# Kernel tuning notes

Hardware: AMD Instinct MI355X
Metric: run time of the kernel (lower is better)

## Reference

```python
import jax, jax.numpy as jnp
import numpy as np

NB, D, H, DH, DHID = 12, 512, 8, 64, 1024  # n_blocks, d_model, n_heads, d_head, d_hidden
B, S = 2, 2048
EPS = 1e-5


def _ln(x, g, b):
    m = jnp.mean(x, axis=-1, keepdims=True)
    v = jnp.mean(jnp.square(x - m), axis=-1, keepdims=True)
    return (x - m) / jnp.sqrt(v + EPS) * g + b


def setup_inputs() -> dict:
    key = jax.random.key(0)
    ks = jax.random.split(key, 8)
    s = 0.02
    f32 = jnp.float32
    return {
        "X": jax.random.normal(ks[0], (B, S, D), f32),
        "qkv_w": jax.random.normal(ks[1], (NB, D, 3 * D), f32) * s,
        "qkv_b": jnp.zeros((NB, 3 * D), f32),
        "fc_w": jax.random.normal(ks[2], (NB, D, D), f32) * s,
        "fc_b": jnp.zeros((NB, D), f32),
        "ln1_g": jnp.ones((NB, D), f32),
        "ln1_b": jnp.zeros((NB, D), f32),
        "w1": jax.random.normal(ks[3], (NB, D, DHID), f32) * s,
        "b1": jnp.zeros((NB, DHID), f32),
        "w2": jax.random.normal(ks[4], (NB, DHID, D), f32) * s,
        "b2": jnp.zeros((NB, D), f32),
        "ln2_g": jnp.ones((NB, D), f32),
        "ln2_b": jnp.zeros((NB, D), f32),
    }


def reference(X, qkv_w, qkv_b, fc_w, fc_b, ln1_g, ln1_b, w1, b1, w2, b2, ln2_g, ln2_b):
    scale = 1.0 / np.sqrt(D)  # NOTE: original scales by 1/sqrt(d_model), not 1/sqrt(d_head)

    def body(x, p):
        qw, qb, fw, fb, g1, be1, w1_, bb1, w2_, bb2, g2, be2 = p
        b, s, _ = x.shape
        # qkv -> [b, h, s, 3*dh]; split per-head AFTER head reshape (as in chunk(dim=-1))
        ctx = (x @ qw + qb).reshape(b, s, H, 3 * DH).transpose(0, 2, 1, 3)
        q, k, v = jnp.split(ctx, 3, axis=-1)  # each [b, h, s, dh]
        attn = jax.nn.softmax(jnp.einsum('bhqd,bhkd->bhqk', q, k) * scale, axis=-1)
        o = jnp.einsum('bhqk,bhkd->bhqd', attn, v).transpose(0, 2, 1, 3).reshape(b, s, D)
        x = x + (o @ fw + fb)                      # residual + attn out proj (dropout=0)
        h = jax.nn.relu(_ln(x, g1, be1) @ w1_ + bb1)
        x = x + (h @ w2_ + bb2)                    # residual + MLP
        return _ln(x, g2, be2), None

    out, _ = jax.lax.scan(
        body, X,
        (qkv_w, qkv_b, fc_w, fc_b, ln1_g, ln1_b, w1, b1, w2, b2, ln2_g, ln2_b))
    return out
```

## Files before the change

kernel.cpp:

```cpp
#include <hip/hip_runtime.h>

typedef unsigned short ushort_t;
typedef __attribute__((ext_vector_type(8))) short bf16x8;
typedef __attribute__((ext_vector_type(4))) float f32x4;
typedef __attribute__((ext_vector_type(4))) unsigned short us4;

#define DEV __device__ __forceinline__

DEV ushort_t f2b(float f) {
    union { float f; unsigned u; } x; x.f = f;
    unsigned r = (x.u + 0x7fffu + ((x.u >> 16) & 1u)) >> 16;
    return (ushort_t)r;
}

DEV unsigned cvt_pk_bf16(float lo, float hi) {
    unsigned r;
    asm("v_cvt_pk_bf16_f32 %0, %1, %2" : "=v"(r) : "v"(lo), "v"(hi));
    return r;
}

typedef void __attribute__((address_space(1)))* gp1;
typedef void __attribute__((address_space(3)))* sp3;
DEV void gload_lds16(const void* g, void* l) {
    __builtin_amdgcn_global_load_lds((gp1)g, (sp3)l, 16, 0, 0);
}

__global__ __launch_bounds__(256) void transpose_cvt(
    const float* __restrict__ in, ushort_t* __restrict__ out, int K, int N)
{
    __shared__ float tile[32][33];
    const int nb = blockIdx.z;
    const float* src = in + (size_t)nb * K * N;
    ushort_t* dst = out + (size_t)nb * K * N;
    const int n0 = blockIdx.x * 32, k0 = blockIdx.y * 32;
    const int tx = threadIdx.x & 31, ty = threadIdx.x >> 5;
#pragma unroll
    for (int i = 0; i < 32; i += 8)
        tile[ty + i][tx] = src[(size_t)(k0 + ty + i) * N + n0 + tx];
    __syncthreads();
#pragma unroll
    for (int i = 0; i < 32; i += 8)
        dst[(size_t)(n0 + ty + i) * K + k0 + tx] = f2b(tile[tx][ty + i]);
}

__global__ __launch_bounds__(256) void init_x(
    const float* __restrict__ X, float* __restrict__ xf, ushort_t* __restrict__ xb)
{
    const int i = blockIdx.x * 256 + threadIdx.x;
    const float4 v = ((const float4*)X)[i];
    ((float4*)xf)[i] = v;
    us4 o = { f2b(v.x), f2b(v.y), f2b(v.z), f2b(v.w) };
    ((us4*)xb)[i] = o;
}

enum { EPI_QKV = 0, EPI_RESF32 = 1, EPI_RELUB = 2 };

template<int EPI>
__global__ __launch_bounds__(256, 2) void gemm64(
    const ushort_t* __restrict__ A, const ushort_t* __restrict__ Wt,
    const float* __restrict__ bias, const float* __restrict__ resid,
    float* __restrict__ Cf, ushort_t* __restrict__ Cb,
    ushort_t* __restrict__ Oq, ushort_t* __restrict__ Ok, ushort_t* __restrict__ Ov,
    int M, int N, int K)
{
    __shared__ __align__(16) ushort_t lA[2][64 * 64];
    __shared__ __align__(16) ushort_t lB[2][128 * 64];
    const int nbm = M >> 6;
    const int bm = blockIdx.x % nbm;
    const int bn = blockIdx.x / nbm;
    const int tid = threadIdx.x, lane = tid & 63, w = tid >> 6;
    const int l15 = lane & 15, l4 = lane >> 4;

    f32x4 acc[4][2];
#pragma unroll
    for (int i = 0; i < 4; i++)
#pragma unroll
        for (int j = 0; j < 2; j++) { f32x4 z = {0.f, 0.f, 0.f, 0.f}; acc[i][j] = z; }

    const int srow = tid >> 3;
    const int sch = tid & 7;
    const int swch = sch ^ (srow & 7);
    const ushort_t* Asrc0 = A  + (size_t)(bm * 64 + srow) * K + swch * 8;
    const ushort_t* Asrc1 = A  + (size_t)(bm * 64 + srow + 32) * K + swch * 8;
    const ushort_t* Bsrc0 = Wt + (size_t)(bn * 128 + srow) * K + swch * 8;
    const ushort_t* Bsrc1 = Wt + (size_t)(bn * 128 + srow + 32) * K + swch * 8;
    const ushort_t* Bsrc2 = Wt + (size_t)(bn * 128 + srow + 64) * K + swch * 8;
    const ushort_t* Bsrc3 = Wt + (size_t)(bn * 128 + srow + 96) * K + swch * 8;
    char* lAc = (char*)lA;
    char* lBc = (char*)lB;

#define GE_STAGE(buf, k0) do {                                            \
        gload_lds16(Asrc0 + (k0), lAc + (buf) * 8192  + w * 1024);        \
        gload_lds16(Asrc1 + (k0), lAc + (buf) * 8192  + 4096 + w * 1024); \
        gload_lds16(Bsrc0 + (k0), lBc + (buf) * 16384 + w * 1024);        \
        gload_lds16(Bsrc1 + (k0), lBc + (buf) * 16384 + 4096 + w * 1024); \
        gload_lds16(Bsrc2 + (k0), lBc + (buf) * 16384 + 8192 + w * 1024); \
        gload_lds16(Bsrc3 + (k0), lBc + (buf) * 16384 + 12288 + w * 1024);\
    } while (0)

    GE_STAGE(0, 0);
    __syncthreads();

    const int nIt = K >> 6;
    int cur = 0;
    for (int it = 0; it < nIt; ++it) {
        if (it + 1 < nIt) GE_STAGE(cur ^ 1, (it + 1) * 64);
#pragma unroll
        for (int ks = 0; ks < 2; ks++) {
            bf16x8 af[4], bfr[2];
#pragma unroll
            for (int i = 0; i < 4; i++) {
                const int row = i * 16 + l15;
                af[i] = *(const bf16x8*)(lAc + cur * 8192 + row * 128 +
                                         (((ks * 4 + l4) ^ (row & 7)) << 4));
            }
#pragma unroll
            for (int j = 0; j < 2; j++) {
                const int row = w * 32 + j * 16 + l15;
                bfr[j] = *(const bf16x8*)(lBc + cur * 16384 + row * 128 +
                                          (((ks * 4 + l4) ^ (row & 7)) << 4));
            }
#pragma unroll
            for (int i = 0; i < 4; i++)
#pragma unroll
                for (int j = 0; j < 2; j++)
                    acc[i][j] = __builtin_amdgcn_mfma_f32_16x16x32_bf16(af[i], bfr[j], acc[i][j], 0, 0, 0);
        }
        __syncthreads();
        cur ^= 1;
    }
#undef GE_STAGE

    const int mbase = bm * 64;
    const int nbase = bn * 128 + w * 32;
#pragma unroll
    for (int j = 0; j < 2; j++) {
        const int nf16 = nbase + j * 16;
        const float bv = bias[nf16 + l15];
        if constexpr (EPI == EPI_QKV) {
            const int head = nf16 / 192;
            const int rem = nf16 - head * 192;
            const int part = rem >> 6;
            const int dh = (rem & 63) + l15;
#pragma unroll
            for (int i = 0; i < 4; i++) {
                const int m0 = mbase + i * 16 + l4 * 4;
#pragma unroll
                for (int r = 0; r < 4; r++) {
                    const int m = m0 + r;
                    const int b = m >> 11, s = m & 2047;
                    const float v = acc[i][j][r] + bv;
                    if (part == 0)
                        Oq[((size_t)(b * 8 + head) * 2048 + s) * 64 + dh] = f2b(v);
                    else if (part == 1)
                        Ok[((size_t)(b * 8 + head) * 2048 + s) * 64 + dh] = f2b(v);
                    else
                        Ov[((size_t)(b * 8 + head) * 64 + dh) * 2048 + s] = f2b(v);
                }
            }
        } else if constexpr (EPI == EPI_RESF32) {
#pragma unroll
            for (int i = 0; i < 4; i++) {
                const int m0 = mbase + i * 16 + l4 * 4;
#pragma unroll
                for (int r = 0; r < 4; r++) {
                    const size_t idx = (size_t)(m0 + r) * N + nf16 + l15;
                    Cf[idx] = acc[i][j][r] + bv + resid[idx];
                }
            }
        } else {
#pragma unroll
            for (int i = 0; i < 4; i++) {
                const int m0 = mbase + i * 16 + l4 * 4;
#pragma unroll
                for (int r = 0; r < 4; r++) {
                    const size_t idx = (size_t)(m0 + r) * N + nf16 + l15;
                    const float v = acc[i][j][r] + bv;
                    Cb[idx] = f2b(v > 0.f ? v : 0.f);
                }
            }
        }
    }
}

__global__ __launch_bounds__(256, 2) void flash_attn3(
    const ushort_t* __restrict__ Q, const ushort_t* __restrict__ Kg,
    const ushort_t* __restrict__ Vg, ushort_t* __restrict__ O, float sl2)
{
    __shared__ __align__(16) ushort_t lK[2][64 * 64];
    __shared__ __align__(16) ushort_t lV[2][64 * 64];
    __shared__ __align__(16) ushort_t lP[4][16 * 64];

    const int id = blockIdx.x;
    const int xcd = id & 7, rest = id >> 3;
    const int qt = rest & 31;
    const int bh = xcd + ((rest >> 5) << 3);
    const int tid = threadIdx.x, lane = tid & 63, w = tid >> 6;
    const int l15 = lane & 15, l4 = lane >> 4;
    const int qrow0 = qt * 64 + w * 16;

    const ushort_t* Qb = Q + ((size_t)bh * 2048 + qrow0) * 64;
    bf16x8 qf[2];
#pragma unroll
    for (int ks = 0; ks < 2; ks++)
        qf[ks] = *(const bf16x8*)(Qb + l15 * 64 + ks * 32 + l4 * 8);

    const ushort_t* Kbase = Kg + (size_t)bh * 2048 * 64;
    const ushort_t* Vbase = Vg + (size_t)bh * 64 * 2048;

    float m_run = -100000.f;
    float l_run = 0.f;
    f32x4 oacc[4];
#pragma unroll
    for (int nd = 0; nd < 4; nd++) { f32x4 z = {0.f, 0.f, 0.f, 0.f}; oacc[nd] = z; }

    char* lKc = (char*)lK;
    char* lVc = (char*)lV;
    char* myP = (char*)(lP[w]);

    const int srow8 = lane >> 3;
    const int sch = lane & 7;

#define FA_STAGE(buf, kt) do {                                              \
        const int row0_ = w * 16 + srow8;                                   \
        const int sc0_ = sch ^ (row0_ & 7);                                 \
        gload_lds16(Kbase + (size_t)((kt) * 64 + row0_) * 64 + sc0_ * 8,    \
                    lKc + (buf) * 8192 + w * 2048);                         \
        gload_lds16(Vbase + (size_t)row0_ * 2048 + (kt) * 64 + sc0_ * 8,    \
                    lVc + (buf) * 8192 + w * 2048);                         \
        gload_lds16(Kbase + (size_t)((kt) * 64 + row0_ + 8) * 64 + sc0_ * 8,\
                    lKc + (buf) * 8192 + w * 2048 + 1024);                  \
        gload_lds16(Vbase + (size_t)(row0_ + 8) * 2048 + (kt) * 64 + sc0_ * 8,\
                    lVc + (buf) * 8192 + w * 2048 + 1024);                  \
    } while (0)

    FA_STAGE(0, 0);
    __syncthreads();

    int cur = 0;
    for (int kt = 0; kt < 32; kt++) {
        if (kt < 31) FA_STAGE(cur ^ 1, kt + 1);

        f32x4 sc4[4];
#pragma unroll
        for (int nf = 0; nf < 4; nf++) { f32x4 z = {0.f, 0.f, 0.f, 0.f}; sc4[nf] = z; }
#pragma unroll
        for (int nf = 0; nf < 4; nf++) {
            const int krow = nf * 16 + l15;
#pragma unroll
            for (int ks = 0; ks < 2; ks++) {
                const bf16x8 kf = *(const bf16x8*)(lKc + cur * 8192 + krow * 128 +
                                                   (((ks * 4 + l4) ^ (krow & 7)) << 4));
                sc4[nf] = __builtin_amdgcn_mfma_f32_16x16x32_bf16(kf, qf[ks], sc4[nf], 0, 0, 0);
            }
        }

        float mx = fmaxf(fmaxf(sc4[0][0], sc4[0][1]), fmaxf(sc4[0][2], sc4[0][3]));
#pragma unroll
        for (int nf = 1; nf < 4; nf++)
            mx = fmaxf(mx, fmaxf(fmaxf(sc4[nf][0], sc4[nf][1]),
                                 fmaxf(sc4[nf][2], sc4[nf][3])));
        mx = fmaxf(mx, __shfl_xor(mx, 16));
        mx = fmaxf(mx, __shfl_xor(mx, 32));

        const int need = (mx > m_run + 125.f) ? 1 : 0;
        if (__any(need)) {
            const float mn = fmaxf(m_run, mx);
            const float corr = exp2f((m_run - mn) * sl2);
            m_run = mn;
            l_run *= corr;
            float cr[4];
#pragma unroll
            for (int r = 0; r < 4; r++) cr[r] = __shfl(corr, l4 * 4 + r);
#pragma unroll
            for (int nd = 0; nd < 4; nd++)
#pragma unroll
                for (int r = 0; r < 4; r++) oacc[nd][r] *= cr[r];
        }

        const float msl = m_run * sl2;
        float ps = 0.f;
#pragma unroll
        for (int nf = 0; nf < 4; nf++)
#pragma unroll
            for (int r = 0; r < 4; r++) {
                const float p = exp2f(sc4[nf][r] * sl2 - msl);
                sc4[nf][r] = p;
                ps += p;
            }
        l_run += ps;

#pragma unroll
        for (int nf = 0; nf < 4; nf++)
#pragma unroll
            for (int h = 0; h < 2; h++) {
                const unsigned pw = cvt_pk_bf16(sc4[nf][2 * h], sc4[nf][2 * h + 1]);
                const int colb = nf * 32 + l4 * 8 + h * 4;
                *(unsigned*)(myP + l15 * 128 + (colb ^ ((l15 & 7) << 4))) = pw;
            }
        __asm__ volatile("" ::: "memory");

        bf16x8 pa[2];
#pragma unroll
        for (int ks = 0; ks < 2; ks++)
            pa[ks] = *(const bf16x8*)(myP + l15 * 128 +
                                      ((ks * 64 + l4 * 16) ^ ((l15 & 7) << 4)));
#pragma unroll
        for (int ks = 0; ks < 2; ks++)
#pragma unroll
            for (int nd = 0; nd < 4; nd++) {
                const int vrow = nd * 16 + l15;
                const bf16x8 vf = *(const bf16x8*)(lVc + cur * 8192 + vrow * 128 +
                                                   (((ks * 4 + l4) ^ (vrow & 7)) << 4));
                oacc[nd] = __builtin_amdgcn_mfma_f32_16x16x32_bf16(pa[ks], vf, oacc[nd], 0, 0, 0);
            }
        __syncthreads();
        cur ^= 1;
    }
#undef FA_STAGE

    l_run += __shfl_xor(l_run, 16);
    l_run += __shfl_xor(l_run, 32);
    const int bq = bh >> 3, hh = bh & 7;
#pragma unroll
    for (int r = 0; r < 4; r++) {
        const float lr = __shfl(l_run, l4 * 4 + r);
        const float inv = 1.f / lr;
        const int s = qrow0 + l4 * 4 + r;
#pragma unroll
        for (int nd = 0; nd < 4; nd++)
            O[((size_t)(bq * 2048 + s)) * 512 + hh * 64 + nd * 16 + l15] = f2b(oacc[nd][r] * inv);
    }
}

__global__ __launch_bounds__(256) void layernorm512(
    const float* X, const float* __restrict__ g, const float* __restrict__ bta,
    ushort_t* __restrict__ Yb, float* Yf)
{
    const int row = blockIdx.x * 4 + (threadIdx.x >> 6);
    const int lane = threadIdx.x & 63;
    const float4* xp = (const float4*)(X + (size_t)row * 512);
    const float4 v0 = xp[lane];
    const float4 v1 = xp[lane + 64];
    float s = v0.x + v0.y + v0.z + v0.w + v1.x + v1.y + v1.z + v1.w;
    float s2 = v0.x * v0.x + v0.y * v0.y + v0.z * v0.z + v0.w * v0.w
             + v1.x * v1.x + v1.y * v1.y + v1.z * v1.z + v1.w * v1.w;
#pragma unroll
    for (int m = 1; m < 64; m <<= 1) { s += __shfl_xor(s, m); s2 += __shfl_xor(s2, m); }
    const float mean = s * (1.f / 512.f);
    const float inv = rsqrtf(s2 * (1.f / 512.f) - mean * mean + 1e-5f);
    const float4 g0 = ((const float4*)g)[lane], g1 = ((const float4*)g)[lane + 64];
    const float4 b0 = ((const float4*)bta)[lane], b1 = ((const float4*)bta)[lane + 64];
    float4 y0, y1;
    y0.x = (v0.x - mean) * inv * g0.x + b0.x;
    y0.y = (v0.y - mean) * inv * g0.y + b0.y;
    y0.z = (v0.z - mean) * inv * g0.z + b0.z;
    y0.w = (v0.w - mean) * inv * g0.w + b0.w;
    y1.x = (v1.x - mean) * inv * g1.x + b1.x;
    y1.y = (v1.y - mean) * inv * g1.y + b1.y;
    y1.z = (v1.z - mean) * inv * g1.z + b1.z;
    y1.w = (v1.w - mean) * inv * g1.w + b1.w;
    if (Yf) {
        ((float4*)(Yf + (size_t)row * 512))[lane] = y0;
        ((float4*)(Yf + (size_t)row * 512))[lane + 64] = y1;
    }
    us4 o0 = { f2b(y0.x), f2b(y0.y), f2b(y0.z), f2b(y0.w) };
    us4 o1 = { f2b(y1.x), f2b(y1.y), f2b(y1.z), f2b(y1.w) };
    ((us4*)(Yb + (size_t)row * 512))[lane] = o0;
    ((us4*)(Yb + (size_t)row * 512))[lane + 64] = o1;
}

extern "C" void kernel_launch(void* const* d_in, const int* in_sizes, int n_in,
                              void* d_out, int out_size, void* d_ws, size_t ws_size,
                              hipStream_t stream)
{
    (void)in_sizes; (void)n_in; (void)out_size; (void)ws_size;
    const float* X     = (const float*)d_in[0];
    const float* qkv_w = (const float*)d_in[1];
    const float* qkv_b = (const float*)d_in[2];
    const float* fc_w  = (const float*)d_in[3];
    const float* fc_b  = (const float*)d_in[4];
    const float* ln1_g = (const float*)d_in[5];
    const float* ln1_b = (const float*)d_in[6];
    const float* w1    = (const float*)d_in[7];
    const float* b1    = (const float*)d_in[8];
    const float* w2    = (const float*)d_in[9];
    const float* b2    = (const float*)d_in[10];
    const float* ln2_g = (const float*)d_in[11];
    const float* ln2_b = (const float*)d_in[12];

    char* ws = (char*)d_ws;
    size_t off = 0;
    auto alloc = [&](size_t bytes) -> char* {
        char* p = ws + off;
        off += (bytes + 255) & ~(size_t)255;
        return p;
    };
    ushort_t* qkvw_t = (ushort_t*)alloc(12ull * 1536 * 512 * 2);
    ushort_t* fcw_t  = (ushort_t*)alloc(12ull * 512 * 512 * 2);
    ushort_t* w1_t   = (ushort_t*)alloc(12ull * 512 * 1024 * 2);
    ushort_t* w2_t   = (ushort_t*)alloc(12ull * 1024 * 512 * 2);
    float*    xf     = (float*)   alloc(4096ull * 512 * 4);
    ushort_t* xb     = (ushort_t*)alloc(4096ull * 512 * 2);
    ushort_t* qb     = (ushort_t*)alloc(16ull * 2048 * 64 * 2);
    ushort_t* kb     = (ushort_t*)alloc(16ull * 2048 * 64 * 2);
    ushort_t* vt     = (ushort_t*)alloc(16ull * 64 * 2048 * 2);
    ushort_t* ob     = (ushort_t*)alloc(4096ull * 512 * 2);
    ushort_t* y1     = (ushort_t*)alloc(4096ull * 512 * 2);
    ushort_t* hbuf   = (ushort_t*)alloc(4096ull * 1024 * 2);

    transpose_cvt<<<dim3(48, 16, 12), 256, 0, stream>>>(qkv_w, qkvw_t, 512, 1536);
    transpose_cvt<<<dim3(16, 16, 12), 256, 0, stream>>>(fc_w, fcw_t, 512, 512);
    transpose_cvt<<<dim3(32, 16, 12), 256, 0, stream>>>(w1, w1_t, 512, 1024);
    transpose_cvt<<<dim3(16, 32, 12), 256, 0, stream>>>(w2, w2_t, 1024, 512);
    init_x<<<2048, 256, 0, stream>>>(X, xf, xb);

    const float sl2 = (float)(0.044194173824159216 * 1.4426950408889634);
    for (int nb = 0; nb < 12; nb++) {
        gemm64<EPI_QKV><<<64 * 12, 256, 0, stream>>>(
            xb, qkvw_t + (size_t)nb * 1536 * 512, qkv_b + nb * 1536,
            nullptr, nullptr, nullptr, qb, kb, vt, 4096, 1536, 512);
        flash_attn3<<<512, 256, 0, stream>>>(qb, kb, vt, ob, sl2);
        gemm64<EPI_RESF32><<<64 * 4, 256, 0, stream>>>(
            ob, fcw_t + (size_t)nb * 512 * 512, fc_b + nb * 512,
            xf, xf, nullptr, nullptr, nullptr, nullptr, 4096, 512, 512);
        layernorm512<<<1024, 256, 0, stream>>>(xf, ln1_g + nb * 512, ln1_b + nb * 512, y1, nullptr);
        gemm64<EPI_RELUB><<<64 * 8, 256, 0, stream>>>(
            y1, w1_t + (size_t)nb * 1024 * 512, b1 + nb * 1024,
            nullptr, nullptr, hbuf, nullptr, nullptr, nullptr, 4096, 1024, 512);
        gemm64<EPI_RESF32><<<64 * 4, 256, 0, stream>>>(
            hbuf, w2_t + (size_t)nb * 1024 * 512, b2 + nb * 512,
            xf, xf, nullptr, nullptr, nullptr, nullptr, 4096, 512, 1024);
        layernorm512<<<1024, 256, 0, stream>>>(xf, ln2_g + nb * 512, ln2_b + nb * 512, xb,
                                               nb == 11 ? (float*)d_out : xf);
    }
}
```

Before: 1.337 ms.

## Split-K residual GEMMs with atomics and double query tiles per wave in attention

The out-projection and MLP-down GEMMs now split K in two across blocks and accumulate into the residual buffer with atomicAdd, with the bias added only by the first split. This doubles the number of blocks for the narrow N=512 GEMMs. Flash attention is restructured so each of 2 waves processes 32 query rows, reusing each K/V LDS fragment for two MFMAs, and gains setprio hints around the matmul sections. The V-transpose store in the QKV epilogue is vectorized. The trade-offs are atomic traffic and nondeterministic summation order, plus fewer waves per attention block.

```diff
diff --git a/kernel.cpp b/kernel.cpp
--- a/kernel.cpp
+++ b/kernel.cpp
@@ -53,12 +53,12 @@
     ((us4*)xb)[i] = o;
 }
 
-enum { EPI_QKV = 0, EPI_RESF32 = 1, EPI_RELUB = 2 };
-
-template<int EPI>
+enum { EPI_QKV = 0, EPI_RESADD = 1, EPI_RELUB = 2 };
+
+template<int EPI, int KSPL>
 __global__ __launch_bounds__(256, 2) void gemm64(
     const ushort_t* __restrict__ A, const ushort_t* __restrict__ Wt,
-    const float* __restrict__ bias, const float* __restrict__ resid,
+    const float* __restrict__ bias,
     float* __restrict__ Cf, ushort_t* __restrict__ Cb,
     ushort_t* __restrict__ Oq, ushort_t* __restrict__ Ok, ushort_t* __restrict__ Ov,
     int M, int N, int K)
@@ -66,8 +66,13 @@
     __shared__ __align__(16) ushort_t lA[2][64 * 64];
     __shared__ __align__(16) ushort_t lB[2][128 * 64];
     const int nbm = M >> 6;
-    const int bm = blockIdx.x % nbm;
-    const int bn = blockIdx.x / nbm;
+    const int nbn = N >> 7;
+    int bid = blockIdx.x;
+    const int bm = bid % nbm; bid /= nbm;
+    const int bn = bid % nbn;
+    const int kh = bid / nbn;
+    const int Keff = K / KSPL;
+    const int kbase = kh * Keff;
     const int tid = threadIdx.x, lane = tid & 63, w = tid >> 6;
     const int l15 = lane & 15, l4 = lane >> 4;
 
@@ -80,12 +85,12 @@
     const int srow = tid >> 3;
     const int sch = tid & 7;
     const int swch = sch ^ (srow & 7);
-    const ushort_t* Asrc0 = A  + (size_t)(bm * 64 + srow) * K + swch * 8;
-    const ushort_t* Asrc1 = A  + (size_t)(bm * 64 + srow + 32) * K + swch * 8;
-    const ushort_t* Bsrc0 = Wt + (size_t)(bn * 128 + srow) * K + swch * 8;
-    const ushort_t* Bsrc1 = Wt + (size_t)(bn * 128 + srow + 32) * K + swch * 8;
-    const ushort_t* Bsrc2 = Wt + (size_t)(bn * 128 + srow + 64) * K + swch * 8;
-    const ushort_t* Bsrc3 = Wt + (size_t)(bn * 128 + srow + 96) * K + swch * 8;
+    const ushort_t* Asrc0 = A  + (size_t)(bm * 64 + srow) * K + kbase + swch * 8;
+    const ushort_t* Asrc1 = A  + (size_t)(bm * 64 + srow + 32) * K + kbase + swch * 8;
+    const ushort_t* Bsrc0 = Wt + (size_t)(bn * 128 + srow) * K + kbase + swch * 8;
+    const ushort_t* Bsrc1 = Wt + (size_t)(bn * 128 + srow + 32) * K + kbase + swch * 8;
+    const ushort_t* Bsrc2 = Wt + (size_t)(bn * 128 + srow + 64) * K + kbase + swch * 8;
+    const ushort_t* Bsrc3 = Wt + (size_t)(bn * 128 + srow + 96) * K + kbase + swch * 8;
     char* lAc = (char*)lA;
     char* lBc = (char*)lB;
 
@@ -101,7 +106,7 @@
     GE_STAGE(0, 0);
     __syncthreads();
 
-    const int nIt = K >> 6;
+    const int nIt = Keff >> 6;
     int cur = 0;
     for (int it = 0; it < nIt; ++it) {
         if (it + 1 < nIt) GE_STAGE(cur ^ 1, (it + 1) * 64);
@@ -145,27 +150,30 @@
 #pragma unroll
             for (int i = 0; i < 4; i++) {
                 const int m0 = mbase + i * 16 + l4 * 4;
-#pragma unroll
-                for (int r = 0; r < 4; r++) {
-                    const int m = m0 + r;
-                    const int b = m >> 11, s = m & 2047;
-                    const float v = acc[i][j][r] + bv;
-                    if (part == 0)
-                        Oq[((size_t)(b * 8 + head) * 2048 + s) * 64 + dh] = f2b(v);
-                    else if (part == 1)
-                        Ok[((size_t)(b * 8 + head) * 2048 + s) * 64 + dh] = f2b(v);
-                    else
-                        Ov[((size_t)(b * 8 + head) * 64 + dh) * 2048 + s] = f2b(v);
+                const int b = m0 >> 11, s0 = m0 & 2047;
+                if (part == 2) {
+                    us4 pv;
+#pragma unroll
+                    for (int r = 0; r < 4; r++) pv[r] = f2b(acc[i][j][r] + bv);
+                    *(us4*)(&Ov[((size_t)(b * 8 + head) * 64 + dh) * 2048 + s0]) = pv;
+                } else {
+                    ushort_t* dst = (part == 0) ? Oq : Ok;
+#pragma unroll
+                    for (int r = 0; r < 4; r++)
+                        dst[((size_t)(b * 8 + head) * 2048 + s0 + r) * 64 + dh] =
+                            f2b(acc[i][j][r] + bv);
                 }
             }
-        } else if constexpr (EPI == EPI_RESF32) {
+        } else if constexpr (EPI == EPI_RESADD) {
+            const float badd = (kh == 0) ? bv : 0.f;
 #pragma unroll
             for (int i = 0; i < 4; i++) {
                 const int m0 = mbase + i * 16 + l4 * 4;
 #pragma unroll
                 for (int r = 0; r < 4; r++) {
                     const size_t idx = (size_t)(m0 + r) * N + nf16 + l15;
-                    Cf[idx] = acc[i][j][r] + bv + resid[idx];
+                    if constexpr (KSPL == 1) Cf[idx] += acc[i][j][r] + badd;
+                    else atomicAdd(&Cf[idx], acc[i][j][r] + badd);
                 }
             }
         } else {
@@ -183,13 +191,13 @@
     }
 }
 
-__global__ __launch_bounds__(256, 2) void flash_attn3(
+__global__ __launch_bounds__(128, 2) void flash_attn4(
     const ushort_t* __restrict__ Q, const ushort_t* __restrict__ Kg,
     const ushort_t* __restrict__ Vg, ushort_t* __restrict__ O, float sl2)
 {
     __shared__ __align__(16) ushort_t lK[2][64 * 64];
     __shared__ __align__(16) ushort_t lV[2][64 * 64];
-    __shared__ __align__(16) ushort_t lP[4][16 * 64];
+    __shared__ __align__(16) ushort_t lP[2][32 * 64];
 
     const int id = blockIdx.x;
     const int xcd = id & 7, rest = id >> 3;
@@ -197,42 +205,42 @@
     const int bh = xcd + ((rest >> 5) << 3);
     const int tid = threadIdx.x, lane = tid & 63, w = tid >> 6;
     const int l15 = lane & 15, l4 = lane >> 4;
-    const int qrow0 = qt * 64 + w * 16;
+    const int qrow0 = qt * 64 + w * 32;
 
     const ushort_t* Qb = Q + ((size_t)bh * 2048 + qrow0) * 64;
-    bf16x8 qf[2];
-#pragma unroll
-    for (int ks = 0; ks < 2; ks++)
-        qf[ks] = *(const bf16x8*)(Qb + l15 * 64 + ks * 32 + l4 * 8);
+    bf16x8 qf[2][2];
+#pragma unroll
+    for (int qi = 0; qi < 2; qi++)
+#pragma unroll
+        for (int ks = 0; ks < 2; ks++)
+            qf[qi][ks] = *(const bf16x8*)(Qb + (qi * 16 + l15) * 64 + ks * 32 + l4 * 8);
 
     const ushort_t* Kbase = Kg + (size_t)bh * 2048 * 64;
     const ushort_t* Vbase = Vg + (size_t)bh * 64 * 2048;
 
-    float m_run = -100000.f;
-    float l_run = 0.f;
-    f32x4 oacc[4];
-#pragma unroll
-    for (int nd = 0; nd < 4; nd++) { f32x4 z = {0.f, 0.f, 0.f, 0.f}; oacc[nd] = z; }
+    float m_run[2] = { -100000.f, -100000.f };
+    float l_run[2] = { 0.f, 0.f };
+    f32x4 oacc[2][4];
+#pragma unroll
+    for (int qi = 0; qi < 2; qi++)
+#pragma unroll
+        for (int nd = 0; nd < 4; nd++) { f32x4 z = {0.f, 0.f, 0.f, 0.f}; oacc[qi][nd] = z; }
 
     char* lKc = (char*)lK;
     char* lVc = (char*)lV;
     char* myP = (char*)(lP[w]);
 
-    const int srow8 = lane >> 3;
-    const int sch = lane & 7;
-
-#define FA_STAGE(buf, kt) do {                                              \
-        const int row0_ = w * 16 + srow8;                                   \
-        const int sc0_ = sch ^ (row0_ & 7);                                 \
-        gload_lds16(Kbase + (size_t)((kt) * 64 + row0_) * 64 + sc0_ * 8,    \
-                    lKc + (buf) * 8192 + w * 2048);                         \
-        gload_lds16(Vbase + (size_t)row0_ * 2048 + (kt) * 64 + sc0_ * 8,    \
-                    lVc + (buf) * 8192 + w * 2048);                         \
-        gload_lds16(Kbase + (size_t)((kt) * 64 + row0_ + 8) * 64 + sc0_ * 8,\
-                    lKc + (buf) * 8192 + w * 2048 + 1024);                  \
-        gload_lds16(Vbase + (size_t)(row0_ + 8) * 2048 + (kt) * 64 + sc0_ * 8,\
-                    lVc + (buf) * 8192 + w * 2048 + 1024);                  \
-    } while (0)
+    const int srow0 = w * 32 + (lane >> 3);
+    const int swch = (lane & 7) ^ (srow0 & 7);
+
+#define FA_STAGE(buf, kt) do {                                                   \
+        _Pragma("unroll")                                                        \
+        for (int i_ = 0; i_ < 4; i_++) {                                         \
+            gload_lds16(Kbase + (size_t)((kt) * 64 + srow0 + i_ * 8) * 64 + swch * 8, \
+                        lKc + (buf) * 8192 + w * 4096 + i_ * 1024);              \
+            gload_lds16(Vbase + (size_t)(srow0 + i_ * 8) * 2048 + (kt) * 64 + swch * 8, \
+                        lVc + (buf) * 8192 + w * 4096 + i_ * 1024);              \
+        } } while (0)
 
     FA_STAGE(0, 0);
     __syncthreads();
@@ -241,9 +249,12 @@
     for (int kt = 0; kt < 32; kt++) {
         if (kt < 31) FA_STAGE(cur ^ 1, kt + 1);
 
-        f32x4 sc4[4];
-#pragma unroll
-        for (int nf = 0; nf < 4; nf++) { f32x4 z = {0.f, 0.f, 0.f, 0.f}; sc4[nf] = z; }
+        f32x4 sc[2][4];
+#pragma unroll
+        for (int qi = 0; qi < 2; qi++)
+#pragma unroll
+            for (int nf = 0; nf < 4; nf++) { f32x4 z = {0.f, 0.f, 0.f, 0.f}; sc[qi][nf] = z; }
+        __builtin_amdgcn_s_setprio(1);
 #pragma unroll
         for (int nf = 0; nf < 4; nf++) {
             const int krow = nf * 16 + l15;
@@ -251,60 +262,84 @@
             for (int ks = 0; ks < 2; ks++) {
                 const bf16x8 kf = *(const bf16x8*)(lKc + cur * 8192 + krow * 128 +
                                                    (((ks * 4 + l4) ^ (krow & 7)) << 4));
-                sc4[nf] = __builtin_amdgcn_mfma_f32_16x16x32_bf16(kf, qf[ks], sc4[nf], 0, 0, 0);
-            }
-        }
-
-        float mx = fmaxf(fmaxf(sc4[0][0], sc4[0][1]), fmaxf(sc4[0][2], sc4[0][3]));
-#pragma unroll
-        for (int nf = 1; nf < 4; nf++)
-            mx = fmaxf(mx, fmaxf(fmaxf(sc4[nf][0], sc4[nf][1]),
-                                 fmaxf(sc4[nf][2], sc4[nf][3])));
-        mx = fmaxf(mx, __shfl_xor(mx, 16));
-        mx = fmaxf(mx, __shfl_xor(mx, 32));
-
-        const int need = (mx > m_run + 125.f) ? 1 : 0;
+                sc[0][nf] = __builtin_amdgcn_mfma_f32_16x16x32_bf16(kf, qf[0][ks], sc[0][nf], 0, 0, 0);
+                sc[1][nf] = __builtin_amdgcn_mfma_f32_16x16x32_bf16(kf, qf[1][ks], sc[1][nf], 0, 0, 0);
+            }
+        }
+        __builtin_amdgcn_s_setprio(0);
+
+        float mx[2];
+#pragma unroll
+        for (int qi = 0; qi < 2; qi++) {
+            float m0 = fmaxf(fmaxf(sc[qi][0][0], sc[qi][0][1]),
+                             fmaxf(sc[qi][0][2], sc[qi][0][3]));
+#pragma unroll
+            for (int nf = 1; nf < 4; nf++)
+                m0 = fmaxf(m0, fmaxf(fmaxf(sc[qi][nf][0], sc[qi][nf][1]),
+                                     fmaxf(sc[qi][nf][2], sc[qi][nf][3])));
+            m0 = fmaxf(m0, __shfl_xor(m0, 16));
+            m0 = fmaxf(m0, __shfl_xor(m0, 32));
+            mx[qi] = m0;
+        }
+        const int need = (mx[0] > m_run[0] + 125.f) | (mx[1] > m_run[1] + 125.f);
         if (__any(need)) {
-            const float mn = fmaxf(m_run, mx);
-            const float corr = exp2f((m_run - mn) * sl2);
-            m_run = mn;
-            l_run *= corr;
-            float cr[4];
-#pragma unroll
-            for (int r = 0; r < 4; r++) cr[r] = __shfl(corr, l4 * 4 + r);
-#pragma unroll
-            for (int nd = 0; nd < 4; nd++)
-#pragma unroll
-                for (int r = 0; r < 4; r++) oacc[nd][r] *= cr[r];
-        }
-
-        const float msl = m_run * sl2;
-        float ps = 0.f;
-#pragma unroll
-        for (int nf = 0; nf < 4; nf++)
-#pragma unroll
-            for (int r = 0; r < 4; r++) {
-                const float p = exp2f(sc4[nf][r] * sl2 - msl);
-                sc4[nf][r] = p;
-                ps += p;
-            }
-        l_run += ps;
-
-#pragma unroll
-        for (int nf = 0; nf < 4; nf++)
-#pragma unroll
-            for (int h = 0; h < 2; h++) {
-                const unsigned pw = cvt_pk_bf16(sc4[nf][2 * h], sc4[nf][2 * h + 1]);
-                const int colb = nf * 32 + l4 * 8 + h * 4;
-                *(unsigned*)(myP + l15 * 128 + (colb ^ ((l15 & 7) << 4))) = pw;
-            }
+#pragma unroll
+            for (int qi = 0; qi < 2; qi++) {
+                const float mn = fmaxf(m_run[qi], mx[qi]);
+                const float corr = exp2f((m_run[qi] - mn) * sl2);
+                m_run[qi] = mn;
+                l_run[qi] *= corr;
+                float cr[4];
+#pragma unroll
+                for (int r = 0; r < 4; r++) cr[r] = __shfl(corr, l4 * 4 + r);
+#pragma unroll
+                for (int nd = 0; nd < 4; nd++)
+#pragma unroll
+                    for (int r = 0; r < 4; r++) oacc[qi][nd][r] *= cr[r];
+            }
+        }
+#pragma unroll
+        for (int qi = 0; qi < 2; qi++) {
+            const float msl = m_run[qi] * sl2;
+            float ps = 0.f;
+#pragma unroll
+            for (int nf = 0; nf < 4; nf++)
+#pragma unroll
+                for (int r = 0; r < 4; r++) {
+                    const float p = exp2f(sc[qi][nf][r] * sl2 - msl);
+                    sc[qi][nf][r] = p;
+                    ps += p;
+                }
+            l_run[qi] += ps;
+        }
+
+        const int hh0 = (l15 >> 3) & 1;
+#pragma unroll
+        for (int qi = 0; qi < 2; qi++) {
+            const int rowP = qi * 16 + l15;
+            char* rp = myP + rowP * 128;
+            const int swz = (l15 & 7) << 4;
+#pragma unroll
+            for (int nf = 0; nf < 4; nf++) {
+                const unsigned pw0 = cvt_pk_bf16(sc[qi][nf][0], sc[qi][nf][1]);
+                const unsigned pw1 = cvt_pk_bf16(sc[qi][nf][2], sc[qi][nf][3]);
+                const unsigned wA = hh0 ? pw1 : pw0;
+                const unsigned wB = hh0 ? pw0 : pw1;
+                const int cbase = nf * 32 + l4 * 8;
+                *(unsigned*)(rp + ((cbase + hh0 * 4) ^ swz)) = wA;
+                *(unsigned*)(rp + ((cbase + (1 - hh0) * 4) ^ swz)) = wB;
+            }
+        }
         __asm__ volatile("" ::: "memory");
 
-        bf16x8 pa[2];
-#pragma unroll
-        for (int ks = 0; ks < 2; ks++)
-            pa[ks] = *(const bf16x8*)(myP + l15 * 128 +
-                                      ((ks * 64 + l4 * 16) ^ ((l15 & 7) << 4)));
+        bf16x8 pa[2][2];
+#pragma unroll
+        for (int qi = 0; qi < 2; qi++)
+#pragma unroll
+            for (int ks = 0; ks < 2; ks++)
+                pa[qi][ks] = *(const bf16x8*)(myP + (qi * 16 + l15) * 128 +
+                                              ((ks * 64 + l4 * 16) ^ ((l15 & 7) << 4)));
+        __builtin_amdgcn_s_setprio(1);
 #pragma unroll
         for (int ks = 0; ks < 2; ks++)
 #pragma unroll
@@ -312,24 +347,31 @@
                 const int vrow = nd * 16 + l15;
                 const bf16x8 vf = *(const bf16x8*)(lVc + cur * 8192 + vrow * 128 +
                                                    (((ks * 4 + l4) ^ (vrow & 7)) << 4));
-                oacc[nd] = __builtin_amdgcn_mfma_f32_16x16x32_bf16(pa[ks], vf, oacc[nd], 0, 0, 0);
-            }
+                oacc[0][nd] = __builtin_amdgcn_mfma_f32_16x16x32_bf16(pa[0][ks], vf, oacc[0][nd], 0, 0, 0);
+                oacc[1][nd] = __builtin_amdgcn_mfma_f32_16x16x32_bf16(pa[1][ks], vf, oacc[1][nd], 0, 0, 0);
+            }
+        __builtin_amdgcn_s_setprio(0);
         __syncthreads();
         cur ^= 1;
     }
 #undef FA_STAGE
 
-    l_run += __shfl_xor(l_run, 16);
-    l_run += __shfl_xor(l_run, 32);
     const int bq = bh >> 3, hh = bh & 7;
 #pragma unroll
-    for (int r = 0; r < 4; r++) {
-        const float lr = __shfl(l_run, l4 * 4 + r);
-        const float inv = 1.f / lr;
-        const int s = qrow0 + l4 * 4 + r;
-#pragma unroll
-        for (int nd = 0; nd < 4; nd++)
-            O[((size_t)(bq * 2048 + s)) * 512 + hh * 64 + nd * 16 + l15] = f2b(oacc[nd][r] * inv);
+    for (int qi = 0; qi < 2; qi++) {
+        float lr = l_run[qi];
+        lr += __shfl_xor(lr, 16);
+        lr += __shfl_xor(lr, 32);
+#pragma unroll
+        for (int r = 0; r < 4; r++) {
+            const float lv = __shfl(lr, l4 * 4 + r);
+            const float inv = 1.f / lv;
+            const int s = qrow0 + qi * 16 + l4 * 4 + r;
+#pragma unroll
+            for (int nd = 0; nd < 4; nd++)
+                O[((size_t)(bq * 2048 + s)) * 512 + hh * 64 + nd * 16 + l15] =
+                    f2b(oacc[qi][nd][r] * inv);
+        }
     }
 }
 
@@ -417,20 +459,20 @@
 
     const float sl2 = (float)(0.044194173824159216 * 1.4426950408889634);
     for (int nb = 0; nb < 12; nb++) {
-        gemm64<EPI_QKV><<<64 * 12, 256, 0, stream>>>(
+        gemm64<EPI_QKV, 1><<<64 * 12, 256, 0, stream>>>(
             xb, qkvw_t + (size_t)nb * 1536 * 512, qkv_b + nb * 1536,
-            nullptr, nullptr, nullptr, qb, kb, vt, 4096, 1536, 512);
-        flash_attn3<<<512, 256, 0, stream>>>(qb, kb, vt, ob, sl2);
-        gemm64<EPI_RESF32><<<64 * 4, 256, 0, stream>>>(
+            nullptr, nullptr, qb, kb, vt, 4096, 1536, 512);
+        flash_attn4<<<512, 128, 0, stream>>>(qb, kb, vt, ob, sl2);
+        gemm64<EPI_RESADD, 2><<<64 * 4 * 2, 256, 0, stream>>>(
             ob, fcw_t + (size_t)nb * 512 * 512, fc_b + nb * 512,
-            xf, xf, nullptr, nullptr, nullptr, nullptr, 4096, 512, 512);
+            xf, nullptr, nullptr, nullptr, nullptr, 4096, 512, 512);
         layernorm512<<<1024, 256, 0, stream>>>(xf, ln1_g + nb * 512, ln1_b + nb * 512, y1, nullptr);
-        gemm64<EPI_RELUB><<<64 * 8, 256, 0, stream>>>(
+        gemm64<EPI_RELUB, 1><<<64 * 8, 256, 0, stream>>>(
             y1, w1_t + (size_t)nb * 1024 * 512, b1 + nb * 1024,
-            nullptr, nullptr, hbuf, nullptr, nullptr, nullptr, 4096, 1024, 512);
-        gemm64<EPI_RESF32><<<64 * 4, 256, 0, stream>>>(
+            nullptr, hbuf, nullptr, nullptr, nullptr, 4096, 1024, 512);
+        gemm64<EPI_RESADD, 2><<<64 * 4 * 2, 256, 0, stream>>>(
             hbuf, w2_t + (size_t)nb * 1024 * 512, b2 + nb * 512,
-            xf, xf, nullptr, nullptr, nullptr, nullptr, 4096, 512, 1024);
+            xf, nullptr, nullptr, nullptr, nullptr, 4096, 512, 1024);
         layernorm512<<<1024, 256, 0, stream>>>(xf, ln2_g + nb * 512, ln2_b + nb * 512, xb,
                                                nb == 11 ? (float*)d_out : xf);
     }
```

Result: slower. 1.747 ms (+30.6%).

## Split attention KV range with combine pass, use 128x128 GEMM tiles for QKV/FC1

Applied to the files above, without the earlier changes.

Attention now splits the KV sequence in two halves across twice as many blocks, writes fp32 partial outputs plus running max and sum, and merges them in a new combine kernel. The QKV and first MLP GEMMs move to a 128x128 tile kernel with 4x4 MFMA per wave, and the V-transpose stores are vectorised. MFMA sections in attention get raised wave priority, and the P-tile LDS writes are reordered to reduce bank conflicts. The residual GEMMs update the fp32 buffer in place. These changes aim for more attention parallelism and better GEMM data reuse, at the cost of extra partial-result traffic and one more launch per layer.

```diff
diff --git a/kernel.cpp b/kernel.cpp
--- a/kernel.cpp
+++ b/kernel.cpp
@@ -53,14 +53,126 @@
     ((us4*)xb)[i] = o;
 }
 
-enum { EPI_QKV = 0, EPI_RESF32 = 1, EPI_RELUB = 2 };
+enum { EPI_QKV = 0, EPI_RESADD = 1, EPI_RELUB = 2 };
 
 template<int EPI>
-__global__ __launch_bounds__(256, 2) void gemm64(
+__global__ __launch_bounds__(256, 2) void gemm128(
     const ushort_t* __restrict__ A, const ushort_t* __restrict__ Wt,
-    const float* __restrict__ bias, const float* __restrict__ resid,
-    float* __restrict__ Cf, ushort_t* __restrict__ Cb,
+    const float* __restrict__ bias, ushort_t* __restrict__ Cb,
     ushort_t* __restrict__ Oq, ushort_t* __restrict__ Ok, ushort_t* __restrict__ Ov,
+    int M, int N, int K)
+{
+    __shared__ __align__(16) ushort_t lA[2][128 * 64];
+    __shared__ __align__(16) ushort_t lB[2][128 * 64];
+    const int nbm = M >> 7;
+    const int bm = blockIdx.x % nbm;
+    const int bn = blockIdx.x / nbm;
+    const int tid = threadIdx.x, lane = tid & 63, w = tid >> 6;
+    const int wr = w >> 1, wc = w & 1;
+    const int l15 = lane & 15, l4 = lane >> 4;
+
+    f32x4 acc[4][4];
+#pragma unroll
+    for (int i = 0; i < 4; i++)
+#pragma unroll
+        for (int j = 0; j < 4; j++) { f32x4 z = {0.f, 0.f, 0.f, 0.f}; acc[i][j] = z; }
+
+    const int srow = tid >> 3;
+    const int sch = tid & 7;
+    const int swch = sch ^ (srow & 7);
+    const ushort_t* As[4];
+    const ushort_t* Bs[4];
+#pragma unroll
+    for (int i = 0; i < 4; i++) {
+        As[i] = A  + (size_t)(bm * 128 + srow + i * 32) * K + swch * 8;
+        Bs[i] = Wt + (size_t)(bn * 128 + srow + i * 32) * K + swch * 8;
+    }
+    char* lAc = (char*)lA;
+    char* lBc = (char*)lB;
+
+#define GE_STAGE(buf, k0) do {                                              \
+        _Pragma("unroll")                                                   \
+        for (int i_ = 0; i_ < 4; i_++) {                                    \
+            gload_lds16(As[i_] + (k0), lAc + (buf) * 16384 + i_ * 4096 + w * 1024); \
+            gload_lds16(Bs[i_] + (k0), lBc + (buf) * 16384 + i_ * 4096 + w * 1024); \
+        } } while (0)
+
+    GE_STAGE(0, 0);
+    __syncthreads();
+
+    const int nIt = K >> 6;
+    int cur = 0;
+    for (int it = 0; it < nIt; ++it) {
+        if (it + 1 < nIt) GE_STAGE(cur ^ 1, (it + 1) * 64);
+#pragma unroll
+        for (int ks = 0; ks < 2; ks++) {
+            bf16x8 af[4], bfr[4];
+#pragma unroll
+            for (int i = 0; i < 4; i++) {
+                const int rowa = wr * 64 + i * 16 + l15;
+                af[i] = *(const bf16x8*)(lAc + cur * 16384 + rowa * 128 +
+                                         (((ks * 4 + l4) ^ (rowa & 7)) << 4));
+                const int rowb = wc * 64 + i * 16 + l15;
+                bfr[i] = *(const bf16x8*)(lBc + cur * 16384 + rowb * 128 +
+                                          (((ks * 4 + l4) ^ (rowb & 7)) << 4));
+            }
+#pragma unroll
+            for (int i = 0; i < 4; i++)
+#pragma unroll
+                for (int j = 0; j < 4; j++)
+                    acc[i][j] = __builtin_amdgcn_mfma_f32_16x16x32_bf16(af[i], bfr[j], acc[i][j], 0, 0, 0);
+        }
+        __syncthreads();
+        cur ^= 1;
+    }
+#undef GE_STAGE
+
+    const int mbase = bm * 128 + wr * 64;
+    const int nbase = bn * 128 + wc * 64;
+#pragma unroll
+    for (int j = 0; j < 4; j++) {
+        const int nf16 = nbase + j * 16;
+        const float bv = bias[nf16 + l15];
+        if constexpr (EPI == EPI_QKV) {
+            const int head = nf16 / 192;
+            const int rem = nf16 - head * 192;
+            const int part = rem >> 6;
+            const int dh = (rem & 63) + l15;
+#pragma unroll
+            for (int i = 0; i < 4; i++) {
+                const int m0 = mbase + i * 16 + l4 * 4;
+                const int b = m0 >> 11, s0 = m0 & 2047;
+                if (part == 2) {
+                    us4 pv;
+#pragma unroll
+                    for (int r = 0; r < 4; r++) pv[r] = f2b(acc[i][j][r] + bv);
+                    *(us4*)(&Ov[((size_t)(b * 8 + head) * 64 + dh) * 2048 + s0]) = pv;
+                } else {
+                    ushort_t* dst = (part == 0) ? Oq : Ok;
+#pragma unroll
+                    for (int r = 0; r < 4; r++)
+                        dst[((size_t)(b * 8 + head) * 2048 + s0 + r) * 64 + dh] =
+                            f2b(acc[i][j][r] + bv);
+                }
+            }
+        } else {
+#pragma unroll
+            for (int i = 0; i < 4; i++) {
+                const int m0 = mbase + i * 16 + l4 * 4;
+#pragma unroll
+                for (int r = 0; r < 4; r++) {
+                    const size_t idx = (size_t)(m0 + r) * N + nf16 + l15;
+                    const float v = acc[i][j][r] + bv;
+                    Cb[idx] = f2b(v > 0.f ? v : 0.f);
+                }
+            }
+        }
+    }
+}
+
+__global__ __launch_bounds__(256, 2) void gemm64_res(
+    const ushort_t* __restrict__ A, const ushort_t* __restrict__ Wt,
+    const float* __restrict__ bias, float* __restrict__ Cf,
     int M, int N, int K)
 {
     __shared__ __align__(16) ushort_t lA[2][64 * 64];
@@ -137,64 +249,32 @@
     for (int j = 0; j < 2; j++) {
         const int nf16 = nbase + j * 16;
         const float bv = bias[nf16 + l15];
-        if constexpr (EPI == EPI_QKV) {
-            const int head = nf16 / 192;
-            const int rem = nf16 - head * 192;
-            const int part = rem >> 6;
-            const int dh = (rem & 63) + l15;
-#pragma unroll
-            for (int i = 0; i < 4; i++) {
-                const int m0 = mbase + i * 16 + l4 * 4;
-#pragma unroll
-                for (int r = 0; r < 4; r++) {
-                    const int m = m0 + r;
-                    const int b = m >> 11, s = m & 2047;
-                    const float v = acc[i][j][r] + bv;
-                    if (part == 0)
-                        Oq[((size_t)(b * 8 + head) * 2048 + s) * 64 + dh] = f2b(v);
-                    else if (part == 1)
-                        Ok[((size_t)(b * 8 + head) * 2048 + s) * 64 + dh] = f2b(v);
-                    else
-                        Ov[((size_t)(b * 8 + head) * 64 + dh) * 2048 + s] = f2b(v);
-                }
-            }
-        } else if constexpr (EPI == EPI_RESF32) {
-#pragma unroll
-            for (int i = 0; i < 4; i++) {
-                const int m0 = mbase + i * 16 + l4 * 4;
-#pragma unroll
-                for (int r = 0; r < 4; r++) {
-                    const size_t idx = (size_t)(m0 + r) * N + nf16 + l15;
-                    Cf[idx] = acc[i][j][r] + bv + resid[idx];
-                }
-            }
-        } else {
-#pragma unroll
-            for (int i = 0; i < 4; i++) {
-                const int m0 = mbase + i * 16 + l4 * 4;
-#pragma unroll
-                for (int r = 0; r < 4; r++) {
-                    const size_t idx = (size_t)(m0 + r) * N + nf16 + l15;
-                    const float v = acc[i][j][r] + bv;
-                    Cb[idx] = f2b(v > 0.f ? v : 0.f);
-                }
-            }
-        }
-    }
-}
-
-__global__ __launch_bounds__(256, 2) void flash_attn3(
+#pragma unroll
+        for (int i = 0; i < 4; i++) {
+            const int m0 = mbase + i * 16 + l4 * 4;
+#pragma unroll
+            for (int r = 0; r < 4; r++) {
+                const size_t idx = (size_t)(m0 + r) * N + nf16 + l15;
+                Cf[idx] += acc[i][j][r] + bv;
+            }
+        }
+    }
+}
+
+__global__ __launch_bounds__(256, 2) void flash_attn5(
     const ushort_t* __restrict__ Q, const ushort_t* __restrict__ Kg,
-    const ushort_t* __restrict__ Vg, ushort_t* __restrict__ O, float sl2)
+    const ushort_t* __restrict__ Vg, float* __restrict__ Opart,
+    float2* __restrict__ ml, float sl2)
 {
     __shared__ __align__(16) ushort_t lK[2][64 * 64];
     __shared__ __align__(16) ushort_t lV[2][64 * 64];
     __shared__ __align__(16) ushort_t lP[4][16 * 64];
 
     const int id = blockIdx.x;
-    const int xcd = id & 7, rest = id >> 3;
-    const int qt = rest & 31;
-    const int bh = xcd + ((rest >> 5) << 3);
+    const int rest = id >> 3;
+    const int kvh = rest & 1;
+    const int qt = (rest >> 1) & 31;
+    const int bh = (id & 7) + ((rest >> 6) << 3);
     const int tid = threadIdx.x, lane = tid & 63, w = tid >> 6;
     const int l15 = lane & 15, l4 = lane >> 4;
     const int qrow0 = qt * 64 + w * 16;
@@ -234,16 +314,18 @@
                     lVc + (buf) * 8192 + w * 2048 + 1024);                  \
     } while (0)
 
-    FA_STAGE(0, 0);
+    const int kt0 = kvh * 16;
+    FA_STAGE(0, kt0);
     __syncthreads();
 
     int cur = 0;
-    for (int kt = 0; kt < 32; kt++) {
-        if (kt < 31) FA_STAGE(cur ^ 1, kt + 1);
+    for (int it = 0; it < 16; it++) {
+        if (it < 15) FA_STAGE(cur ^ 1, kt0 + it + 1);
 
         f32x4 sc4[4];
 #pragma unroll
         for (int nf = 0; nf < 4; nf++) { f32x4 z = {0.f, 0.f, 0.f, 0.f}; sc4[nf] = z; }
+        __builtin_amdgcn_s_setprio(1);
 #pragma unroll
         for (int nf = 0; nf < 4; nf++) {
             const int krow = nf * 16 + l15;
@@ -254,6 +336,7 @@
                 sc4[nf] = __builtin_amdgcn_mfma_f32_16x16x32_bf16(kf, qf[ks], sc4[nf], 0, 0, 0);
             }
         }
+        __builtin_amdgcn_s_setprio(0);
 
         float mx = fmaxf(fmaxf(sc4[0][0], sc4[0][1]), fmaxf(sc4[0][2], sc4[0][3]));
 #pragma unroll
@@ -290,14 +373,21 @@
             }
         l_run += ps;
 
-#pragma unroll
-        for (int nf = 0; nf < 4; nf++)
-#pragma unroll
-            for (int h = 0; h < 2; h++) {
-                const unsigned pw = cvt_pk_bf16(sc4[nf][2 * h], sc4[nf][2 * h + 1]);
-                const int colb = nf * 32 + l4 * 8 + h * 4;
-                *(unsigned*)(myP + l15 * 128 + (colb ^ ((l15 & 7) << 4))) = pw;
-            }
+        const int hh0 = (l15 >> 3) & 1;
+        {
+            char* rp = myP + l15 * 128;
+            const int swz = (l15 & 7) << 4;
+#pragma unroll
+            for (int nf = 0; nf < 4; nf++) {
+                const unsigned pw0 = cvt_pk_bf16(sc4[nf][0], sc4[nf][1]);
+                const unsigned pw1 = cvt_pk_bf16(sc4[nf][2], sc4[nf][3]);
+                const unsigned wA = hh0 ? pw1 : pw0;
+                const unsigned wB = hh0 ? pw0 : pw1;
+                const int cbase = nf * 32 + l4 * 8;
+                *(unsigned*)(rp + ((cbase + hh0 * 4) ^ swz)) = wA;
+                *(unsigned*)(rp + ((cbase + (1 - hh0) * 4) ^ swz)) = wB;
+            }
+        }
         __asm__ volatile("" ::: "memory");
 
         bf16x8 pa[2];
@@ -305,6 +395,7 @@
         for (int ks = 0; ks < 2; ks++)
             pa[ks] = *(const bf16x8*)(myP + l15 * 128 +
                                       ((ks * 64 + l4 * 16) ^ ((l15 & 7) << 4)));
+        __builtin_amdgcn_s_setprio(1);
 #pragma unroll
         for (int ks = 0; ks < 2; ks++)
 #pragma unroll
@@ -314,6 +405,7 @@
                                                    (((ks * 4 + l4) ^ (vrow & 7)) << 4));
                 oacc[nd] = __builtin_amdgcn_mfma_f32_16x16x32_bf16(pa[ks], vf, oacc[nd], 0, 0, 0);
             }
+        __builtin_amdgcn_s_setprio(0);
         __syncthreads();
         cur ^= 1;
     }
@@ -321,16 +413,42 @@
 
     l_run += __shfl_xor(l_run, 16);
     l_run += __shfl_xor(l_run, 32);
-    const int bq = bh >> 3, hh = bh & 7;
-#pragma unroll
-    for (int r = 0; r < 4; r++) {
-        const float lr = __shfl(l_run, l4 * 4 + r);
-        const float inv = 1.f / lr;
-        const int s = qrow0 + l4 * 4 + r;
+    float* Op = Opart + ((size_t)(kvh * 16 + bh) * 2048 + qrow0) * 64;
+#pragma unroll
+    for (int r = 0; r < 4; r++)
 #pragma unroll
         for (int nd = 0; nd < 4; nd++)
-            O[((size_t)(bq * 2048 + s)) * 512 + hh * 64 + nd * 16 + l15] = f2b(oacc[nd][r] * inv);
-    }
+            Op[(size_t)(l4 * 4 + r) * 64 + nd * 16 + l15] = oacc[nd][r];
+    if (lane < 16) {
+        float2 v; v.x = m_run; v.y = l_run;
+        ml[(size_t)(kvh * 16 + bh) * 2048 + qrow0 + lane] = v;
+    }
+}
+
+__global__ __launch_bounds__(256) void combine_attn(
+    const float* __restrict__ Opart, const float2* __restrict__ ml,
+    ushort_t* __restrict__ O, float sl2)
+{
+    const int gid = blockIdx.x * 256 + threadIdx.x;
+    const int d4 = (gid & 15) * 4;
+    const int s = (gid >> 4) & 2047;
+    const int bh = gid >> 15;
+    const float4 o0 = *(const float4*)(Opart + ((size_t)bh * 2048 + s) * 64 + d4);
+    const float4 o1 = *(const float4*)(Opart + ((size_t)(16 + bh) * 2048 + s) * 64 + d4);
+    const float2 ml0 = ml[(size_t)bh * 2048 + s];
+    const float2 ml1 = ml[(size_t)(16 + bh) * 2048 + s];
+    const float m = fmaxf(ml0.x, ml1.x);
+    const float w0 = exp2f((ml0.x - m) * sl2);
+    const float w1 = exp2f((ml1.x - m) * sl2);
+    const float inv = 1.f / (ml0.y * w0 + ml1.y * w1);
+    us4 out;
+    out[0] = f2b((o0.x * w0 + o1.x * w1) * inv);
+    out[1] = f2b((o0.y * w0 + o1.y * w1) * inv);
+    out[2] = f2b((o0.z * w0 + o1.z * w1) * inv);
+    out[3] = f2b((o0.w * w0 + o1.w * w1) * inv);
+    const int row = (bh >> 3) * 2048 + s;
+    const int col = (bh & 7) * 64 + d4;
+    *(us4*)(&O[(size_t)row * 512 + col]) = out;
 }
 
 __global__ __launch_bounds__(256) void layernorm512(
@@ -408,6 +526,8 @@
     ushort_t* ob     = (ushort_t*)alloc(4096ull * 512 * 2);
     ushort_t* y1     = (ushort_t*)alloc(4096ull * 512 * 2);
     ushort_t* hbuf   = (ushort_t*)alloc(4096ull * 1024 * 2);
+    float*    opart  = (float*)   alloc(32ull * 2048 * 64 * 4);
+    float2*   mlbuf  = (float2*)  alloc(32ull * 2048 * 8);
 
     transpose_cvt<<<dim3(48, 16, 12), 256, 0, stream>>>(qkv_w, qkvw_t, 512, 1536);
     transpose_cvt<<<dim3(16, 16, 12), 256, 0, stream>>>(fc_w, fcw_t, 512, 512);
@@ -417,20 +537,19 @@
 
     const float sl2 = (float)(0.044194173824159216 * 1.4426950408889634);
     for (int nb = 0; nb < 12; nb++) {
-        gemm64<EPI_QKV><<<64 * 12, 256, 0, stream>>>(
+        gemm128<EPI_QKV><<<32 * 12, 256, 0, stream>>>(
             xb, qkvw_t + (size_t)nb * 1536 * 512, qkv_b + nb * 1536,
-            nullptr, nullptr, nullptr, qb, kb, vt, 4096, 1536, 512);
-        flash_attn3<<<512, 256, 0, stream>>>(qb, kb, vt, ob, sl2);
-        gemm64<EPI_RESF32><<<64 * 4, 256, 0, stream>>>(
-            ob, fcw_t + (size_t)nb * 512 * 512, fc_b + nb * 512,
-            xf, xf, nullptr, nullptr, nullptr, nullptr, 4096, 512, 512);
+            nullptr, qb, kb, vt, 4096, 1536, 512);
+        flash_attn5<<<1024, 256, 0, stream>>>(qb, kb, vt, opart, mlbuf, sl2);
+        combine_attn<<<2048, 256, 0, stream>>>(opart, mlbuf, ob, sl2);
+        gemm64_res<<<64 * 4, 256, 0, stream>>>(
+            ob, fcw_t + (size_t)nb * 512 * 512, fc_b + nb * 512, xf, 4096, 512, 512);
         layernorm512<<<1024, 256, 0, stream>>>(xf, ln1_g + nb * 512, ln1_b + nb * 512, y1, nullptr);
-        gemm64<EPI_RELUB><<<64 * 8, 256, 0, stream>>>(
+        gemm128<EPI_RELUB><<<32 * 8, 256, 0, stream>>>(
             y1, w1_t + (size_t)nb * 1024 * 512, b1 + nb * 1024,
-            nullptr, nullptr, hbuf, nullptr, nullptr, nullptr, 4096, 1024, 512);
-        gemm64<EPI_RESF32><<<64 * 4, 256, 0, stream>>>(
-            hbuf, w2_t + (size_t)nb * 1024 * 512, b2 + nb * 512,
-            xf, xf, nullptr, nullptr, nullptr, nullptr, 4096, 512, 1024);
+            hbuf, nullptr, nullptr, nullptr, 4096, 1024, 512);
+        gemm64_res<<<64 * 4, 256, 0, stream>>>(
+            hbuf, w2_t + (size_t)nb * 1024 * 512, b2 + nb * 512, xf, 4096, 512, 1024);
         layernorm512<<<1024, 256, 0, stream>>>(xf, ln2_g + nb * 512, ln2_b + nb * 512, xb,
                                                nb == 11 ? (float*)d_out : xf);
     }
```

Result: slower. 1.404 ms (+5.0%).
